# Optimization experiments

Measured on AMD Instinct MI355X. Metric: run time of the kernel, lower is better.

## Reference

```python
import jax, jax.numpy as jnp
import numpy as np

B = 262144
NUM_CLASSES = 1000
K = 4
CODE_DIM = 256


def setup_inputs() -> dict:
    key = jax.random.key(0)
    k1, k2, k3 = jax.random.split(key, 3)
    codes = jax.random.uniform(k1, (B, CODE_DIM), dtype=jnp.float32)
    pred_class = jax.random.randint(k2, (B,), 0, NUM_CLASSES, dtype=jnp.int64)
    centroids = jax.random.uniform(k3, (NUM_CLASSES, K, CODE_DIM), dtype=jnp.float32)
    return {"codes": codes, "pred_class": pred_class, "centroids": centroids}


def reference(codes, pred_class, centroids):
    # Gather the k centroids of each sample's predicted class: [B, K, D]
    cents = centroids[pred_class]
    # Mean absolute (normalized Hamming-style) distance per centroid: [B, K]
    d = jnp.mean(jnp.abs(codes[:, None, :] - cents), axis=2)
    # Min over the k centroids -> [B]
    return jnp.min(d, axis=1)
```

## Files before the change

### kernel.cpp

```cpp
#include <hip/hip_runtime.h>


#define B_TOTAL     262144
#define NUM_CLASSES 1000
#define KC          4
#define DIM         256

__global__ __launch_bounds__(256) void sparse_codebook_kernel(
    const float* __restrict__ codes,
    const int*   __restrict__ pred_class,
    const float* __restrict__ centroids,
    float*       __restrict__ out)
{
    const int tid    = blockIdx.x * blockDim.x + threadIdx.x;
    const int sample = tid >> 6;
    const int lane   = threadIdx.x & 63;
    if (sample >= B_TOTAL) return;

    const int cls = __builtin_amdgcn_readfirstlane(pred_class[sample]);

    const float4* codes4 = (const float4*)codes + (size_t)sample * 64;
    const float4  c      = codes4[lane];

    const float4* cent4 = (const float4*)centroids + (size_t)cls * (KC * DIM / 4);

    float s[KC];
#pragma unroll
    for (int k = 0; k < KC; ++k) {
        const float4 g = cent4[k * 64 + lane];
        s[k] = fabsf(c.x - g.x) + fabsf(c.y - g.y)
             + fabsf(c.z - g.z) + fabsf(c.w - g.w);
    }

#pragma unroll
    for (int off = 32; off > 0; off >>= 1) {
#pragma unroll
        for (int k = 0; k < KC; ++k)
            s[k] += __shfl_xor(s[k], off, 64);
    }

    if (lane == 0) {
        const float m = fminf(fminf(s[0], s[1]), fminf(s[2], s[3]));
        out[sample] = m * (1.0f / (float)DIM);
    }
}

extern "C" void kernel_launch(void* const* d_in, const int* in_sizes, int n_in,
                              void* d_out, int out_size, void* d_ws, size_t ws_size,
                              hipStream_t stream) {
    const float* codes = (const float*)d_in[0];
    const int*   pred  = (const int*)d_in[1];
    const float* cents = (const float*)d_in[2];
    float*       out   = (float*)d_out;

    const int total_threads = B_TOTAL * 64;
    const int block = 256;
    const int grid  = total_threads / block;
    sparse_codebook_kernel<<<grid, block, 0, stream>>>(codes, pred, cents, out);
}
```

Baseline: 366.7 us.

## Counting-sort samples by class before distance kernel for centroid locality

Adds a histogram, a prefix scan and a scatter pass that produce a permutation grouping samples by predicted class. The main kernel then visits samples in class order, so consecutive waves reuse the same centroid rows in cache. In exchange it adds three extra launches, a memset and atomics, and reads of codes and writes of outputs become scattered. A direct fallback path remains for when the workspace is too small.

```diff
diff --git a/kernel.cpp b/kernel.cpp
--- a/kernel.cpp
+++ b/kernel.cpp
@@ -6,18 +6,58 @@
 #define KC          4
 #define DIM         256
 
-__global__ __launch_bounds__(256) void sparse_codebook_kernel(
+#define WS_NEEDED   ((size_t)(2048 + B_TOTAL) * sizeof(int))
+
+__global__ __launch_bounds__(256) void hist_kernel(
+    const int* __restrict__ pred, int* __restrict__ counts)
+{
+    const int i = blockIdx.x * 256 + threadIdx.x;
+    if (i < B_TOTAL) atomicAdd(&counts[pred[i]], 1);
+}
+
+__global__ __launch_bounds__(1024) void scan_kernel(
+    const int* __restrict__ counts, int* __restrict__ cursors)
+{
+    __shared__ int sc[1024];
+    const int i = threadIdx.x;
+    const int v = (i < NUM_CLASSES) ? counts[i] : 0;
+    sc[i] = v;
+    __syncthreads();
+#pragma unroll
+    for (int off = 1; off < 1024; off <<= 1) {
+        const int t = (i >= off) ? sc[i - off] : 0;
+        __syncthreads();
+        sc[i] += t;
+        __syncthreads();
+    }
+    if (i < NUM_CLASSES) cursors[i] = sc[i] - v;
+}
+
+__global__ __launch_bounds__(256) void scatter_kernel(
+    const int* __restrict__ pred, int* __restrict__ cursors,
+    int* __restrict__ sorted)
+{
+    const int i = blockIdx.x * 256 + threadIdx.x;
+    if (i < B_TOTAL) {
+        const int c   = pred[i];
+        const int pos = atomicAdd(&cursors[c], 1);
+        sorted[pos] = i;
+    }
+}
+
+__global__ __launch_bounds__(256) void sparse_codebook_sorted(
     const float* __restrict__ codes,
     const int*   __restrict__ pred_class,
     const float* __restrict__ centroids,
+    const int*   __restrict__ sorted,
     float*       __restrict__ out)
 {
-    const int tid    = blockIdx.x * blockDim.x + threadIdx.x;
-    const int sample = tid >> 6;
-    const int lane   = threadIdx.x & 63;
-    if (sample >= B_TOTAL) return;
+    const int p    = (blockIdx.x * 256 + threadIdx.x) >> 6;
+    const int lane = threadIdx.x & 63;
+    if (p >= B_TOTAL) return;
 
-    const int cls = __builtin_amdgcn_readfirstlane(pred_class[sample]);
+    const int sample = __builtin_amdgcn_readfirstlane(sorted[p]);
+    const int cls    = __builtin_amdgcn_readfirstlane(pred_class[sample]);
 
     const float4* codes4 = (const float4*)codes + (size_t)sample * 64;
     const float4  c      = codes4[lane];
@@ -45,6 +85,37 @@
     }
 }
 
+__global__ __launch_bounds__(256) void sparse_codebook_direct(
+    const float* __restrict__ codes,
+    const int*   __restrict__ pred_class,
+    const float* __restrict__ centroids,
+    float*       __restrict__ out)
+{
+    const int sample = (blockIdx.x * 256 + threadIdx.x) >> 6;
+    const int lane   = threadIdx.x & 63;
+    if (sample >= B_TOTAL) return;
+
+    const int cls = __builtin_amdgcn_readfirstlane(pred_class[sample]);
+    const float4 c = ((const float4*)codes + (size_t)sample * 64)[lane];
+    const float4* cent4 = (const float4*)centroids + (size_t)cls * (KC * DIM / 4);
+
+    float s[KC];
+#pragma unroll
+    for (int k = 0; k < KC; ++k) {
+        const float4 g = cent4[k * 64 + lane];
+        s[k] = fabsf(c.x - g.x) + fabsf(c.y - g.y)
+             + fabsf(c.z - g.z) + fabsf(c.w - g.w);
+    }
+#pragma unroll
+    for (int off = 32; off > 0; off >>= 1)
+#pragma unroll
+        for (int k = 0; k < KC; ++k)
+            s[k] += __shfl_xor(s[k], off, 64);
+
+    if (lane == 0)
+        out[sample] = fminf(fminf(s[0], s[1]), fminf(s[2], s[3])) * (1.0f / (float)DIM);
+}
+
 extern "C" void kernel_launch(void* const* d_in, const int* in_sizes, int n_in,
                               void* d_out, int out_size, void* d_ws, size_t ws_size,
                               hipStream_t stream) {
@@ -53,8 +124,20 @@
     const float* cents = (const float*)d_in[2];
     float*       out   = (float*)d_out;
 
-    const int total_threads = B_TOTAL * 64;
-    const int block = 256;
-    const int grid  = total_threads / block;
-    sparse_codebook_kernel<<<grid, block, 0, stream>>>(codes, pred, cents, out);
+    if (ws_size >= WS_NEEDED) {
+        int* counts  = (int*)d_ws;
+        int* cursors = counts + 1024;
+        int* sorted  = counts + 2048;
+
+        hipMemsetAsync(counts, 0, 1024 * sizeof(int), stream);
+        hist_kernel   <<<(B_TOTAL + 255) / 256, 256, 0, stream>>>(pred, counts);
+        scan_kernel   <<<1, 1024, 0, stream>>>(counts, cursors);
+        scatter_kernel<<<(B_TOTAL + 255) / 256, 256, 0, stream>>>(pred, cursors, sorted);
+
+        const int grid = (B_TOTAL * 64) / 256;
+        sparse_codebook_sorted<<<grid, 256, 0, stream>>>(codes, pred, cents, sorted, out);
+    } else {
+        const int grid = (B_TOTAL * 64) / 256;
+        sparse_codebook_direct<<<grid, 256, 0, stream>>>(codes, pred, cents, out);
+    }
 }
```

Measured after the change: 499.6 us. +36.2%, slower.

## Process four samples per wavefront with 16-lane groups and nontemporal code loads

Applied to the files above, without the earlier changes.

Each wavefront now handles four samples, one per 16-lane quarter. Each lane loads four float4 code chunks and sixteen centroid chunks, so the shuffle reduction shrinks from six steps to four. Code rows are read with nontemporal loads so they do not evict the reused centroids from cache. In exchange, the class id is no longer wave-uniform, so centroid addresses become per-lane gathers, and per-thread register use goes up.

```diff
diff --git a/kernel.cpp b/kernel.cpp
--- a/kernel.cpp
+++ b/kernel.cpp
@@ -6,42 +6,55 @@
 #define KC          4
 #define DIM         256
 
-__global__ __launch_bounds__(256) void sparse_codebook_kernel(
+typedef float vf4 __attribute__((ext_vector_type(4)));
+
+__global__ __launch_bounds__(256) void sparse_codebook_q4(
     const float* __restrict__ codes,
     const int*   __restrict__ pred_class,
     const float* __restrict__ centroids,
     float*       __restrict__ out)
 {
-    const int tid    = blockIdx.x * blockDim.x + threadIdx.x;
-    const int sample = tid >> 6;
-    const int lane   = threadIdx.x & 63;
-    if (sample >= B_TOTAL) return;
+    const int wave = (blockIdx.x * 256 + threadIdx.x) >> 6;
+    const int lane = threadIdx.x & 63;
+    const int q    = lane >> 4;
+    const int l    = lane & 15;
+    const int s0   = wave * 4;
+    if (s0 >= B_TOTAL) return;
 
-    const int cls = __builtin_amdgcn_readfirstlane(pred_class[sample]);
+    const int my_sample = s0 + q;
+    const int cls = pred_class[my_sample];
 
-    const float4* codes4 = (const float4*)codes + (size_t)sample * 64;
-    const float4  c      = codes4[lane];
+    const vf4* crow = (const vf4*)codes + (size_t)my_sample * 64;
+    vf4 c[4];
+#pragma unroll
+    for (int j = 0; j < 4; ++j)
+        c[j] = __builtin_nontemporal_load(&crow[j * 16 + l]);
 
-    const float4* cent4 = (const float4*)centroids + (size_t)cls * (KC * DIM / 4);
+    const vf4* cbase = (const vf4*)centroids + (size_t)cls * (KC * DIM / 4);
 
     float s[KC];
 #pragma unroll
     for (int k = 0; k < KC; ++k) {
-        const float4 g = cent4[k * 64 + lane];
-        s[k] = fabsf(c.x - g.x) + fabsf(c.y - g.y)
-             + fabsf(c.z - g.z) + fabsf(c.w - g.w);
+        float acc = 0.0f;
+#pragma unroll
+        for (int j = 0; j < 4; ++j) {
+            const vf4 g = cbase[k * 16 * 4 + j * 16 + l];
+            acc += fabsf(c[j].x - g.x) + fabsf(c[j].y - g.y)
+                 + fabsf(c[j].z - g.z) + fabsf(c[j].w - g.w);
+        }
+        s[k] = acc;
     }
 
 #pragma unroll
-    for (int off = 32; off > 0; off >>= 1) {
+    for (int off = 8; off >= 1; off >>= 1) {
 #pragma unroll
         for (int k = 0; k < KC; ++k)
             s[k] += __shfl_xor(s[k], off, 64);
     }
 
-    if (lane == 0) {
+    if (l == 0) {
         const float m = fminf(fminf(s[0], s[1]), fminf(s[2], s[3]));
-        out[sample] = m * (1.0f / (float)DIM);
+        out[my_sample] = m * (1.0f / (float)DIM);
     }
 }
 
@@ -53,8 +66,8 @@
     const float* cents = (const float*)d_in[2];
     float*       out   = (float*)d_out;
 
-    const int total_threads = B_TOTAL * 64;
+    const int total_threads = B_TOTAL * 16;
     const int block = 256;
     const int grid  = total_threads / block;
-    sparse_codebook_kernel<<<grid, block, 0, stream>>>(codes, pred, cents, out);
+    sparse_codebook_q4<<<grid, block, 0, stream>>>(codes, pred, cents, out);
 }
```

Result: slower. 376.6 us (+2.7%).
